# Kernel optimization log

Measured on AMD Instinct MI355X. Metric: run time of the kernel, lower is better.

The kernel has to match this reference:

```python
import jax, jax.numpy as jnp
import numpy as np

B, C, CI, H, W = 8, 128, 64, 64, 64  # batch, in_channels, inter_channels, spatial


def setup_inputs() -> dict:
    key = jax.random.key(0)
    ks = jax.random.split(key, 9)
    s_in = 1.0 / np.sqrt(C)
    s_ci = 1.0 / np.sqrt(CI)
    return {
        "x": jax.random.normal(ks[0], (B, C, H, W), dtype=jnp.float32),
        # 1x1 conv weights stored as [out, in] (kernel dims squeezed)
        "g_w": jax.random.uniform(ks[1], (CI, C), jnp.float32, -s_in, s_in),
        "g_b": jax.random.uniform(ks[2], (CI,), jnp.float32, -s_in, s_in),
        "theta_w": jax.random.uniform(ks[3], (CI, C), jnp.float32, -s_in, s_in),
        "theta_b": jax.random.uniform(ks[4], (CI,), jnp.float32, -s_in, s_in),
        "phi_w": jax.random.uniform(ks[5], (CI, C), jnp.float32, -s_in, s_in),
        "phi_b": jax.random.uniform(ks[6], (CI,), jnp.float32, -s_in, s_in),
        # W is zero-init in the original; use small random values so the
        # output path is exercised (as it would be after training).
        "W_w": jax.random.uniform(ks[7], (C, CI), jnp.float32, -s_ci, s_ci),
        "W_b": jax.random.uniform(ks[8], (C,), jnp.float32, -s_ci, s_ci),
    }


def reference(x, g_w, g_b, theta_w, theta_b, phi_w, phi_b, W_w, W_b):
    b, c, h, w = x.shape
    n = h * w
    xf = x.reshape(b, c, n)  # [B, C, N]

    def conv1x1(wt, bias, inp):  # 1x1 conv over flattened spatial dim
        return jnp.einsum('oi,bin->bon', wt, inp) + bias[None, :, None]

    g_x = conv1x1(g_w, g_b, xf).transpose(0, 2, 1)        # [B, N, CI]
    theta_x = conv1x1(theta_w, theta_b, xf).transpose(0, 2, 1)  # [B, N, CI]
    phi_x = conv1x1(phi_w, phi_b, xf)                     # [B, CI, N]

    f = jnp.einsum('bnc,bcm->bnm', theta_x, phi_x)        # [B, N, N]
    # NOTE: original applies softmax over dim=1 (query axis), faithfully kept.
    f_div_C = jax.nn.softmax(f, axis=1)

    y = jnp.einsum('bnm,bmc->bnc', f_div_C, g_x)          # [B, N, CI]
    y = y.transpose(0, 2, 1)                              # [B, CI, N]
    W_y = conv1x1(W_w, W_b, y)                            # [B, C, N]
    return W_y.reshape(b, c, h, w) + x
```

## Files before the change

kernel.cpp:

```cpp
#include <hip/hip_runtime.h>

#define B_ 8
#define C_ 128
#define CI_ 64
#define N_ 4096

typedef _Float16 f16x8 __attribute__((ext_vector_type(8)));
typedef _Float16 f16x4 __attribute__((ext_vector_type(4)));
typedef float   f32x4  __attribute__((ext_vector_type(4)));


__global__ __launch_bounds__(256) void k_transpose(const float* __restrict__ x,
                                                   _Float16* __restrict__ xT)
{
    __shared__ float tile[64][65];
    int b = blockIdx.z, c0 = blockIdx.y * 64, n0 = blockIdx.x * 64;
    int tx = threadIdx.x & 63, ty = threadIdx.x >> 6;
#pragma unroll
    for (int i = 0; i < 16; i++) {
        int c = ty + i * 4;
        tile[c][tx] = x[((size_t)b * C_ + c0 + c) * N_ + n0 + tx];
    }
    __syncthreads();
#pragma unroll
    for (int i = 0; i < 16; i++) {
        int n = ty + i * 4;
        xT[((size_t)b * N_ + n0 + n) * C_ + c0 + tx] = (_Float16)tile[tx][n];
    }
}

__global__ __launch_bounds__(256) void k_wconv(
    const float* __restrict__ thw, const float* __restrict__ phw,
    const float* __restrict__ gw,  const float* __restrict__ ww,
    _Float16* __restrict__ wTh, _Float16* __restrict__ wPh,
    _Float16* __restrict__ wG,  _Float16* __restrict__ wW)
{
    int i = blockIdx.x * 256 + threadIdx.x;
    int which = i >> 13, j = i & 8191;
    if (which == 0)      wTh[j] = (_Float16)thw[j];
    else if (which == 1) wPh[j] = (_Float16)phw[j];
    else if (which == 2) wG[j]  = (_Float16)gw[j];
    else                 wW[j]  = (_Float16)ww[j];
}

__global__ __launch_bounds__(256) void k_proj(
    const _Float16* __restrict__ xT,
    const _Float16* __restrict__ wTh, const _Float16* __restrict__ wPh,
    const _Float16* __restrict__ wG,
    const float* __restrict__ bTh, const float* __restrict__ bPh,
    const float* __restrict__ bG,
    _Float16* __restrict__ thS, _Float16* __restrict__ phS,
    _Float16* __restrict__ gS)
{
    const float kLog2e = 1.44269504088896f;
    int b = blockIdx.y, n0 = blockIdx.x * 64;
    int tid = threadIdx.x, wave = tid >> 6, lane = tid & 63;
    int l16 = lane & 15, quad = lane >> 4;
    const _Float16* xTb = xT + (size_t)b * N_ * C_;
    const _Float16* aRow = xTb + (size_t)(n0 + wave * 16 + l16) * C_ + quad * 8;

#pragma unroll
    for (int p = 0; p < 2; p++) {
        const _Float16* w = p ? wPh : wTh;
        const float* bias = p ? bPh : bTh;
        _Float16* outp = p ? phS : thS;
        float scale = p ? 1.0f : kLog2e;
        f32x4 acc[4] = {};
#pragma unroll
        for (int kc = 0; kc < 4; kc++) {
            f16x8 a = *(const f16x8*)(aRow + kc * 32);
#pragma unroll
            for (int t = 0; t < 4; t++) {
                f16x8 bb = *(const f16x8*)(w + (size_t)(t * 16 + l16) * C_ + kc * 32 + quad * 8);
                acc[t] = __builtin_amdgcn_mfma_f32_16x16x32_f16(a, bb, acc[t], 0, 0, 0);
            }
        }
#pragma unroll
        for (int t = 0; t < 4; t++) {
            float bv = bias[t * 16 + l16];
            int half = t >> 1;
            int q2 = (t & 1) * 2 + (l16 >> 3);
            int e = l16 & 7;
            size_t base = ((size_t)(b * 256 + (n0 >> 4) + wave) * 2 + half) * 512;
#pragma unroll
            for (int r = 0; r < 4; r++)
                outp[base + (q2 * 16 + quad * 4 + r) * 8 + e] =
                    (_Float16)((acc[t][r] + bv) * scale);
        }
    }
    {
        f32x4 acc[4] = {};
#pragma unroll
        for (int kc = 0; kc < 4; kc++) {
            f16x8 a = *(const f16x8*)(wG + (size_t)(wave * 16 + l16) * C_ + kc * 32 + quad * 8);
#pragma unroll
            for (int t = 0; t < 4; t++) {
                f16x8 bb = *(const f16x8*)(xTb + (size_t)(n0 + t * 16 + l16) * C_ + kc * 32 + quad * 8);
                acc[t] = __builtin_amdgcn_mfma_f32_16x16x32_f16(a, bb, acc[t], 0, 0, 0);
            }
        }
#pragma unroll
        for (int t = 0; t < 4; t++) {
            size_t base = (size_t)(b * 256 + (n0 >> 4) + t) * 1024;
#pragma unroll
            for (int r = 0; r < 4; r++) {
                int ci = wave * 16 + quad * 4 + r;
                gS[base + ((size_t)((l16 >> 2) * 16 + quad * 4 + r)) * 16 + wave * 4 + (l16 & 3)] =
                    (_Float16)(acc[t][r] + bG[ci]);
            }
        }
    }
}

__global__ __launch_bounds__(512) void k_stats(
    const _Float16* __restrict__ thS, const _Float16* __restrict__ phS,
    float* __restrict__ nl2d)
{
    __shared__ float Dp[8][64];
    int b = blockIdx.y, m0 = blockIdx.x * 64;
    int tid = threadIdx.x, wave = tid >> 6, lane = tid & 63;
    int l16 = lane & 15, quad = lane >> 4;

    f16x8 Bp[4][2];
#pragma unroll
    for (int t = 0; t < 4; t++) {
        const _Float16* cb = phS + (size_t)(b * 256 + (m0 >> 4) + t) * 1024 + lane * 8;
        Bp[t][0] = *(const f16x8*)(cb);
        Bp[t][1] = *(const f16x8*)(cb + 512);
    }
    float csum[4] = {0.f, 0.f, 0.f, 0.f};
    const _Float16* pA = thS + (size_t)(b * 256 + wave * 32) * 1024 + lane * 8;
    f16x8 A0 = *(const f16x8*)pA, A1 = *(const f16x8*)(pA + 512);
    for (int nc = 0; nc < 32; nc++) {
        const _Float16* pN = pA + ((nc < 31) ? 1024 : 0);
        f16x8 nA0 = *(const f16x8*)pN, nA1 = *(const f16x8*)(pN + 512);
        pA = pN;
#pragma unroll
        for (int t = 0; t < 4; t++) {
            f32x4 s = {0.f, 0.f, 0.f, 0.f};
            s = __builtin_amdgcn_mfma_f32_16x16x32_f16(A0, Bp[t][0], s, 0, 0, 0);
            s = __builtin_amdgcn_mfma_f32_16x16x32_f16(A1, Bp[t][1], s, 0, 0, 0);
            csum[t] += __builtin_amdgcn_exp2f(s[0]) + __builtin_amdgcn_exp2f(s[1])
                     + __builtin_amdgcn_exp2f(s[2]) + __builtin_amdgcn_exp2f(s[3]);
        }
        A0 = nA0; A1 = nA1;
    }
#pragma unroll
    for (int t = 0; t < 4; t++) {
        float s = csum[t];
        s += __shfl_xor(s, 16);
        s += __shfl_xor(s, 32);
        if (quad == 0) Dp[wave][t * 16 + l16] = s;
    }
    __syncthreads();
    if (tid < 64) {
        float d = Dp[0][tid] + Dp[1][tid] + Dp[2][tid] + Dp[3][tid]
                + Dp[4][tid] + Dp[5][tid] + Dp[6][tid] + Dp[7][tid];
        nl2d[(size_t)b * N_ + m0 + tid] = -__builtin_amdgcn_logf(d);
    }
}

__global__ __launch_bounds__(512) void k_attn(
    const _Float16* __restrict__ thS, const _Float16* __restrict__ phS,
    const _Float16* __restrict__ gS, const float* __restrict__ nl2d,
    _Float16* __restrict__ Yf)
{
    __shared__ float red[4][4096];
    int b = blockIdx.y, n0 = blockIdx.x * 64;
    int tid = threadIdx.x, wave = tid >> 6, lane = tid & 63;
    int l16 = lane & 15, quad = lane >> 4;
    const float* nlb = nl2d + (size_t)b * N_;

    f16x8 Bt[4][2];
#pragma unroll
    for (int nt = 0; nt < 4; nt++) {
        const _Float16* cb = thS + (size_t)(b * 256 + (n0 >> 4) + nt) * 1024 + lane * 8;
        Bt[nt][0] = *(const f16x8*)(cb);
        Bt[nt][1] = *(const f16x8*)(cb + 512);
    }
    f32x4 Y[4][4] = {};

    const _Float16* pA = phS + (size_t)(b * 256 + wave * 32) * 1024 + lane * 8;
    const _Float16* pG = gS  + (size_t)(b * 256 + wave * 32) * 1024 + lane * 16;
    f16x8 A0 = *(const f16x8*)pA, A1 = *(const f16x8*)(pA + 512);
    f16x8 G0 = *(const f16x8*)pG, G1 = *(const f16x8*)(pG + 8);
    f32x4 z = *(const f32x4*)(nlb + wave * 512 + quad * 4);

    for (int mc = 0; mc < 32; mc++) {
        int step = (mc < 31) ? 1024 : 0;
        f16x8 nA0 = *(const f16x8*)(pA + step), nA1 = *(const f16x8*)(pA + step + 512);
        f16x8 nG0 = *(const f16x8*)(pG + step), nG1 = *(const f16x8*)(pG + step + 8);
        f32x4 nz = *(const f32x4*)(nlb + wave * 512 + mc * 16 + (step ? 16 : 0) + quad * 4);
        pA += step; pG += step;

        f32x4 S[4];
#pragma unroll
        for (int nt = 0; nt < 4; nt++) {
            f32x4 acc = z;
            acc = __builtin_amdgcn_mfma_f32_16x16x32_f16(A0, Bt[nt][0], acc, 0, 0, 0);
            S[nt] = __builtin_amdgcn_mfma_f32_16x16x32_f16(A1, Bt[nt][1], acc, 0, 0, 0);
        }
        f16x4 P[4];
#pragma unroll
        for (int nt = 0; nt < 4; nt++)
#pragma unroll
            for (int r = 0; r < 4; r++)
                P[nt][r] = (_Float16)__builtin_amdgcn_exp2f(S[nt][r]);

        f16x4 gf[4];
        gf[0] = __builtin_shufflevector(G0, G0, 0, 1, 2, 3);
        gf[1] = __builtin_shufflevector(G0, G0, 4, 5, 6, 7);
        gf[2] = __builtin_shufflevector(G1, G1, 0, 1, 2, 3);
        gf[3] = __builtin_shufflevector(G1, G1, 4, 5, 6, 7);
#pragma unroll
        for (int ct = 0; ct < 4; ct++)
#pragma unroll
            for (int nt = 0; nt < 4; nt++)
                Y[ct][nt] = __builtin_amdgcn_mfma_f32_16x16x16f16(gf[ct], P[nt], Y[ct][nt], 0, 0, 0);

        A0 = nA0; A1 = nA1; G0 = nG0; G1 = nG1; z = nz;
    }

    if (wave >= 4) {
        float* s = &red[wave - 4][lane * 4];
#pragma unroll
        for (int ct = 0; ct < 4; ct++)
#pragma unroll
            for (int nt = 0; nt < 4; nt++)
                *(f32x4*)(s + (ct * 4 + nt) * 256) = Y[ct][nt];
    }
    __syncthreads();
    if (wave < 4) {
        float* s = &red[wave][lane * 4];
#pragma unroll
        for (int ct = 0; ct < 4; ct++)
#pragma unroll
            for (int nt = 0; nt < 4; nt++) {
                Y[ct][nt] += *(const f32x4*)(s + (ct * 4 + nt) * 256);
                *(f32x4*)(s + (ct * 4 + nt) * 256) = Y[ct][nt];
            }
    }
    __syncthreads();
    {
        int n = tid >> 3, k8 = tid & 7;
        _Float16 vals[8];
#pragma unroll
        for (int j = 0; j < 8; j++) {
            int ci = k8 * 8 + j;
            int ct = ci >> 4, jj = ci & 15, q = jj >> 2, r = jj & 3;
            int idx = (ct * 4 + (n >> 4)) * 256 + (q * 16 + (n & 15)) * 4 + r;
            vals[j] = (_Float16)(red[0][idx] + red[1][idx] + red[2][idx] + red[3][idx]);
        }
        *(f16x8*)(Yf + ((size_t)b * N_ + n0 + n) * CI_ + k8 * 8) = *(f16x8*)vals;
    }
}

__global__ __launch_bounds__(256) void k_out(
    const _Float16* __restrict__ wW, const float* __restrict__ Wb,
    const _Float16* __restrict__ Yf, const float* __restrict__ x,
    float* __restrict__ out)
{
    int b = blockIdx.y, n0 = blockIdx.x * 64;
    int tid = threadIdx.x, wave = tid >> 6, lane = tid & 63;
    int l16 = lane & 15, quad = lane >> 4;
    f16x8 Af[2][2];
#pragma unroll
    for (int rt = 0; rt < 2; rt++)
#pragma unroll
        for (int kc = 0; kc < 2; kc++)
            Af[rt][kc] = *(const f16x8*)(wW + (size_t)(wave * 32 + rt * 16 + l16) * CI_ + kc * 32 + quad * 8);
    f32x4 acc[2][4] = {};
#pragma unroll
    for (int t = 0; t < 4; t++) {
        const _Float16* yp = Yf + ((size_t)b * N_ + n0 + t * 16 + l16) * CI_;
        f16x8 b0 = *(const f16x8*)(yp + quad * 8);
        f16x8 b1 = *(const f16x8*)(yp + 32 + quad * 8);
#pragma unroll
        for (int rt = 0; rt < 2; rt++) {
            acc[rt][t] = __builtin_amdgcn_mfma_f32_16x16x32_f16(Af[rt][0], b0, acc[rt][t], 0, 0, 0);
            acc[rt][t] = __builtin_amdgcn_mfma_f32_16x16x32_f16(Af[rt][1], b1, acc[rt][t], 0, 0, 0);
        }
    }
#pragma unroll
    for (int rt = 0; rt < 2; rt++)
#pragma unroll
        for (int t = 0; t < 4; t++)
#pragma unroll
            for (int r = 0; r < 4; r++) {
                int c = wave * 32 + rt * 16 + quad * 4 + r;
                size_t o = ((size_t)b * C_ + c) * N_ + n0 + t * 16 + l16;
                out[o] = acc[rt][t][r] + Wb[c] + x[o];
            }
}

extern "C" void kernel_launch(void* const* d_in, const int* in_sizes, int n_in,
                              void* d_out, int out_size, void* d_ws, size_t ws_size,
                              hipStream_t stream)
{
    const float* x    = (const float*)d_in[0];
    const float* g_w  = (const float*)d_in[1];
    const float* g_b  = (const float*)d_in[2];
    const float* th_w = (const float*)d_in[3];
    const float* th_b = (const float*)d_in[4];
    const float* ph_w = (const float*)d_in[5];
    const float* ph_b = (const float*)d_in[6];
    const float* W_w  = (const float*)d_in[7];
    const float* W_b  = (const float*)d_in[8];
    float* out = (float*)d_out;

    char* ws = (char*)d_ws;
    _Float16* xT  = (_Float16*)(ws);
    _Float16* thS = (_Float16*)(ws + 8388608);
    _Float16* phS = (_Float16*)(ws + 12582912);
    _Float16* gS  = (_Float16*)(ws + 16777216);
    _Float16* Yf  = (_Float16*)(ws + 20971520);
    float*    nl2d= (float*)   (ws + 25165824);
    _Float16* wTh = (_Float16*)(ws + 25296896);
    _Float16* wPh = (_Float16*)(ws + 25313280);
    _Float16* wG  = (_Float16*)(ws + 25329664);
    _Float16* wW  = (_Float16*)(ws + 25346048);

    hipLaunchKernelGGL(k_transpose, dim3(64, 2, 8), dim3(256), 0, stream, x, xT);
    hipLaunchKernelGGL(k_wconv, dim3(128), dim3(256), 0, stream,
                       th_w, ph_w, g_w, W_w, wTh, wPh, wG, wW);
    hipLaunchKernelGGL(k_proj, dim3(64, 8), dim3(256), 0, stream,
                       xT, wTh, wPh, wG, th_b, ph_b, g_b, thS, phS, gS);
    hipLaunchKernelGGL(k_stats, dim3(64, 8), dim3(512), 0, stream, thS, phS, nl2d);
    hipLaunchKernelGGL(k_attn, dim3(64, 8), dim3(512), 0, stream, thS, phS, gS, nl2d, Yf);
    hipLaunchKernelGGL(k_out, dim3(64, 8), dim3(256), 0, stream, wW, W_b, Yf, x, out);
}
```

Before: 179.8 us.

## Software-pipeline stats exp with MFMA; shrink attn LDS to fp16 and raise occupancy

```diff
diff --git a/kernel.cpp b/kernel.cpp
--- a/kernel.cpp
+++ b/kernel.cpp
@@ -128,26 +128,57 @@
         Bp[t][0] = *(const f16x8*)(cb);
         Bp[t][1] = *(const f16x8*)(cb + 512);
     }
-    float csum[4] = {0.f, 0.f, 0.f, 0.f};
+    f32x4 csum4[4] = {};
     const _Float16* pA = thS + (size_t)(b * 256 + wave * 32) * 1024 + lane * 8;
     f16x8 A0 = *(const f16x8*)pA, A1 = *(const f16x8*)(pA + 512);
-    for (int nc = 0; nc < 32; nc++) {
+    f32x4 Sp[4];
+    {
+        const _Float16* pN = pA + 1024;
+        f16x8 nA0 = *(const f16x8*)pN, nA1 = *(const f16x8*)(pN + 512);
+        pA = pN;
+#pragma unroll
+        for (int t = 0; t < 4; t++) {
+            f32x4 s = {0.f, 0.f, 0.f, 0.f};
+            s = __builtin_amdgcn_mfma_f32_16x16x32_f16(A0, Bp[t][0], s, 0, 0, 0);
+            Sp[t] = __builtin_amdgcn_mfma_f32_16x16x32_f16(A1, Bp[t][1], s, 0, 0, 0);
+        }
+        A0 = nA0; A1 = nA1;
+    }
+    for (int nc = 1; nc < 32; nc++) {
         const _Float16* pN = pA + ((nc < 31) ? 1024 : 0);
         f16x8 nA0 = *(const f16x8*)pN, nA1 = *(const f16x8*)(pN + 512);
         pA = pN;
+        f32x4 Sc[4];
 #pragma unroll
         for (int t = 0; t < 4; t++) {
             f32x4 s = {0.f, 0.f, 0.f, 0.f};
             s = __builtin_amdgcn_mfma_f32_16x16x32_f16(A0, Bp[t][0], s, 0, 0, 0);
-            s = __builtin_amdgcn_mfma_f32_16x16x32_f16(A1, Bp[t][1], s, 0, 0, 0);
-            csum[t] += __builtin_amdgcn_exp2f(s[0]) + __builtin_amdgcn_exp2f(s[1])
-                     + __builtin_amdgcn_exp2f(s[2]) + __builtin_amdgcn_exp2f(s[3]);
+            Sc[t] = __builtin_amdgcn_mfma_f32_16x16x32_f16(A1, Bp[t][1], s, 0, 0, 0);
+        }
+#pragma unroll
+        for (int t = 0; t < 4; t++) {
+            f32x4 e;
+            e[0] = __builtin_amdgcn_exp2f(Sp[t][0]);
+            e[1] = __builtin_amdgcn_exp2f(Sp[t][1]);
+            e[2] = __builtin_amdgcn_exp2f(Sp[t][2]);
+            e[3] = __builtin_amdgcn_exp2f(Sp[t][3]);
+            csum4[t] += e;
+            Sp[t] = Sc[t];
         }
         A0 = nA0; A1 = nA1;
     }
 #pragma unroll
     for (int t = 0; t < 4; t++) {
-        float s = csum[t];
+        f32x4 e;
+        e[0] = __builtin_amdgcn_exp2f(Sp[t][0]);
+        e[1] = __builtin_amdgcn_exp2f(Sp[t][1]);
+        e[2] = __builtin_amdgcn_exp2f(Sp[t][2]);
+        e[3] = __builtin_amdgcn_exp2f(Sp[t][3]);
+        csum4[t] += e;
+    }
+#pragma unroll
+    for (int t = 0; t < 4; t++) {
+        float s = (csum4[t][0] + csum4[t][1]) + (csum4[t][2] + csum4[t][3]);
         s += __shfl_xor(s, 16);
         s += __shfl_xor(s, 32);
         if (quad == 0) Dp[wave][t * 16 + l16] = s;
@@ -160,12 +191,12 @@
     }
 }
 
-__global__ __launch_bounds__(512) void k_attn(
+__global__ __launch_bounds__(512, 4) void k_attn(
     const _Float16* __restrict__ thS, const _Float16* __restrict__ phS,
     const _Float16* __restrict__ gS, const float* __restrict__ nl2d,
     _Float16* __restrict__ Yf)
 {
-    __shared__ float red[4][4096];
+    __shared__ _Float16 red[4][4096];
     int b = blockIdx.y, n0 = blockIdx.x * 64;
     int tid = threadIdx.x, wave = tid >> 6, lane = tid & 63;
     int l16 = lane & 15, quad = lane >> 4;
@@ -180,18 +211,20 @@
     }
     f32x4 Y[4][4] = {};
 
-    const _Float16* pA = phS + (size_t)(b * 256 + wave * 32) * 1024 + lane * 8;
-    const _Float16* pG = gS  + (size_t)(b * 256 + wave * 32) * 1024 + lane * 16;
+    const int base = b * 256 + wave * 32;
+    const _Float16* pA = phS + (size_t)base * 1024 + lane * 8;
+    const _Float16* pG = gS  + (size_t)base * 1024 + lane * 16;
+    const float*    pZ = nlb + wave * 512 + quad * 4;
+
     f16x8 A0 = *(const f16x8*)pA, A1 = *(const f16x8*)(pA + 512);
-    f16x8 G0 = *(const f16x8*)pG, G1 = *(const f16x8*)(pG + 8);
-    f32x4 z = *(const f32x4*)(nlb + wave * 512 + quad * 4);
+    f32x4 z = *(const f32x4*)pZ;
 
     for (int mc = 0; mc < 32; mc++) {
         int step = (mc < 31) ? 1024 : 0;
+        f16x8 G0 = *(const f16x8*)pG, G1 = *(const f16x8*)(pG + 8);
         f16x8 nA0 = *(const f16x8*)(pA + step), nA1 = *(const f16x8*)(pA + step + 512);
-        f16x8 nG0 = *(const f16x8*)(pG + step), nG1 = *(const f16x8*)(pG + step + 8);
-        f32x4 nz = *(const f32x4*)(nlb + wave * 512 + mc * 16 + (step ? 16 : 0) + quad * 4);
-        pA += step; pG += step;
+        f32x4 nz = *(const f32x4*)(pZ + (step >> 6));
+        pA += step; pG += step; pZ += (step >> 6);
 
         f32x4 S[4];
 #pragma unroll
@@ -218,26 +251,34 @@
             for (int nt = 0; nt < 4; nt++)
                 Y[ct][nt] = __builtin_amdgcn_mfma_f32_16x16x16f16(gf[ct], P[nt], Y[ct][nt], 0, 0, 0);
 
-        A0 = nA0; A1 = nA1; G0 = nG0; G1 = nG1; z = nz;
+        A0 = nA0; A1 = nA1; z = nz;
     }
 
     if (wave >= 4) {
-        float* s = &red[wave - 4][lane * 4];
+        _Float16* s = &red[wave - 4][lane * 4];
 #pragma unroll
         for (int ct = 0; ct < 4; ct++)
 #pragma unroll
-            for (int nt = 0; nt < 4; nt++)
-                *(f32x4*)(s + (ct * 4 + nt) * 256) = Y[ct][nt];
+            for (int nt = 0; nt < 4; nt++) {
+                f16x4 h;
+#pragma unroll
+                for (int r = 0; r < 4; r++) h[r] = (_Float16)Y[ct][nt][r];
+                *(f16x4*)(s + (ct * 4 + nt) * 256) = h;
+            }
     }
     __syncthreads();
     if (wave < 4) {
-        float* s = &red[wave][lane * 4];
+        _Float16* s = &red[wave][lane * 4];
 #pragma unroll
         for (int ct = 0; ct < 4; ct++)
 #pragma unroll
             for (int nt = 0; nt < 4; nt++) {
-                Y[ct][nt] += *(const f32x4*)(s + (ct * 4 + nt) * 256);
-                *(f32x4*)(s + (ct * 4 + nt) * 256) = Y[ct][nt];
+                f16x4 h = *(const f16x4*)(s + (ct * 4 + nt) * 256);
+                f16x4 o;
+#pragma unroll
+                for (int r = 0; r < 4; r++)
+                    o[r] = (_Float16)(Y[ct][nt][r] + (float)h[r]);
+                *(f16x4*)(s + (ct * 4 + nt) * 256) = o;
             }
     }
     __syncthreads();
@@ -249,7 +290,8 @@
             int ci = k8 * 8 + j;
             int ct = ci >> 4, jj = ci & 15, q = jj >> 2, r = jj & 3;
             int idx = (ct * 4 + (n >> 4)) * 256 + (q * 16 + (n & 15)) * 4 + r;
-            vals[j] = (_Float16)(red[0][idx] + red[1][idx] + red[2][idx] + red[3][idx]);
+            vals[j] = (_Float16)(((float)red[0][idx] + (float)red[1][idx])
+                               + ((float)red[2][idx] + (float)red[3][idx]));
         }
         *(f16x8*)(Yf + ((size_t)b * N_ + n0 + n) * CI_ + k8 * 8) = *(f16x8*)vals;
     }
```

After: 180.5 us. About the same (+0.4%).
